# Performance work log

Hardware: AMD Instinct MI355X
Metric: run time of the kernel (lower is better)

Reference implementation:

```python
import jax, jax.numpy as jnp
import numpy as np

N_NODES = 100000
N_EDGES = 1000000
IN_DIM = 128
HID = 128
OUT_DIM = 40


def setup_inputs() -> dict:
    key = jax.random.key(0)
    ks = jax.random.split(key, 16)
    x = jax.random.normal(ks[0], (N_NODES, IN_DIM), dtype=jnp.float32)
    edge_index = jax.random.randint(ks[1], (2, N_EDGES), 0, N_NODES, dtype=jnp.int64)
    s = 0.05
    # GAT layer 1 (in->hid, heads=1, concat=True)
    W1 = jax.random.normal(ks[2], (HID, IN_DIM), jnp.float32) * s
    b1 = jnp.zeros((HID,), jnp.float32)
    att1 = jax.random.normal(ks[3], (1, 2 * HID), jnp.float32) * s
    bias1 = jnp.zeros((HID,), jnp.float32)
    # GAT layer 2 (hid->hid)
    W2 = jax.random.normal(ks[4], (HID, HID), jnp.float32) * s
    b2 = jnp.zeros((HID,), jnp.float32)
    att2 = jax.random.normal(ks[5], (1, 2 * HID), jnp.float32) * s
    bias2 = jnp.zeros((HID,), jnp.float32)
    # post_mp: Linear(hid,hid) -> Dropout -> Linear(hid,out)
    Wp1 = jax.random.normal(ks[6], (HID, HID), jnp.float32) * s
    bp1 = jnp.zeros((HID,), jnp.float32)
    Wp2 = jax.random.normal(ks[7], (OUT_DIM, HID), jnp.float32) * s
    bp2 = jnp.zeros((OUT_DIM,), jnp.float32)
    return dict(x=x, edge_index=edge_index, W1=W1, b1=b1, att1=att1, bias1=bias1,
                W2=W2, b2=b2, att2=att2, bias2=bias2,
                Wp1=Wp1, bp1=bp1, Wp2=Wp2, bp2=bp2)


def gat_layer(x, src, dst, W, b, att, bias, n_nodes):
    # x: [N, Fin] -> h: [N, C] (heads=1, concat=True)
    h = x @ W.T + b
    C = h.shape[1]
    att_i, att_j = att[0, :C], att[0, C:]  # split: first half pairs with x_i (dst), second with x_j (src)
    # per-node scalar projections, then gather per edge (avoids [E,2C] concat)
    e = (h @ att_i)[dst] + (h @ att_j)[src]  # [E]
    e = jnp.where(e > 0, e, 0.2 * e)  # leaky_relu(0.2)
    # segment softmax over destination nodes
    m = jax.ops.segment_max(e, dst, num_segments=n_nodes)
    ex = jnp.exp(e - m[dst])
    denom = jax.ops.segment_sum(ex, dst, num_segments=n_nodes)
    alpha = ex / denom[dst]
    out = jax.ops.segment_sum(h[src] * alpha[:, None], dst, num_segments=n_nodes)
    return out + bias


def reference(x, edge_index, W1, b1, att1, bias1, W2, b2, att2, bias2, Wp1, bp1, Wp2, bp2):
    src, dst = edge_index[0], edge_index[1]
    n = x.shape[0]
    h = jax.nn.relu(gat_layer(x, src, dst, W1, b1, att1, bias1, n))  # dropout p=0 -> identity
    h = jax.nn.relu(gat_layer(h, src, dst, W2, b2, att2, bias2, n))
    y = (h @ Wp1.T + bp1) @ Wp2.T + bp2  # post_mp (eval: dropout identity)
    return jax.nn.log_softmax(y, axis=1)
```

## Files before the change

### kernel.cpp

```cpp
#include <hip/hip_runtime.h>

#define N_NODES 100000
#define N_EDGES 1000000
#define HID 128
#define OUT_DIM 40
#define CSR_W 64
#define CUR_STRIDE 16
#define GEMM_TILES 1563
#define G2_TILES 782
#define PROJ_TILES 1563
#define EDGE_BLK 977
#define WC_BLK 21

typedef __attribute__((ext_vector_type(8))) short bf16x8;
typedef __attribute__((ext_vector_type(4))) float f32x4;

__device__ inline unsigned short f2bf(float f) {
    unsigned u = __float_as_uint(f);
    u += 0x7fffu + ((u >> 16) & 1u);
    return (unsigned short)(u >> 16);
}
__device__ inline float bf2f(unsigned short u) {
    return __uint_as_float(((unsigned)u) << 16);
}

__device__ inline float4 ld4(const float* p) { return *(const float4*)p; }
__device__ inline float4 ld4(const unsigned short* p) {
    ushort4 u = *(const ushort4*)p;
    return make_float4(bf2f(u.x), bf2f(u.y), bf2f(u.z), bf2f(u.w));
}

__global__ __launch_bounds__(256) void zero_kernel(float4* __restrict__ p, int n4) {
    int i = blockIdx.x * 256 + threadIdx.x;
    int stride = gridDim.x * 256;
    float4 z = make_float4(0.f, 0.f, 0.f, 0.f);
    for (; i < n4; i += stride) p[i] = z;
}

#define LDA 136
template<typename AT>
__device__ __forceinline__ void gemm_tile_body(
    int tile, const AT* __restrict__ A, const float* __restrict__ W,
    const float* __restrict__ out_bias, const float* __restrict__ in_bias,
    int relu_in, const float* __restrict__ att,
    unsigned short* __restrict__ Cb, float* __restrict__ hi, float* __restrict__ hj,
    int n_rows, unsigned short* As, unsigned short* Ws)
{
    const int t = threadIdx.x;
    const int row0 = tile * 64;

    for (int i = 0; i < 8; i++) {
        int lin = t + i * 256;
        int r = lin >> 5;
        int k = (lin & 31) * 4;
        int gr = row0 + r;
        float4 av = make_float4(0.f, 0.f, 0.f, 0.f);
        if (gr < n_rows) av = ld4(A + (size_t)gr * HID + k);
        if (in_bias) {
            av.x += in_bias[k + 0]; av.y += in_bias[k + 1];
            av.z += in_bias[k + 2]; av.w += in_bias[k + 3];
            if (relu_in) {
                av.x = fmaxf(av.x, 0.f); av.y = fmaxf(av.y, 0.f);
                av.z = fmaxf(av.z, 0.f); av.w = fmaxf(av.w, 0.f);
            }
        }
        ushort4 bv;
        bv.x = f2bf(av.x); bv.y = f2bf(av.y); bv.z = f2bf(av.z); bv.w = f2bf(av.w);
        *(ushort4*)(&As[r * LDA + k]) = bv;
    }
    for (int i = 0; i < 16; i++) {
        int lin = t + i * 256;
        int r = lin >> 5;
        int k = (lin & 31) * 4;
        float4 wv = *(const float4*)(W + (size_t)r * HID + k);
        ushort4 bv;
        bv.x = f2bf(wv.x); bv.y = f2bf(wv.y); bv.z = f2bf(wv.z); bv.w = f2bf(wv.w);
        *(ushort4*)(&Ws[r * LDA + k]) = bv;
    }
    __syncthreads();

    const int wave = t >> 6, lane = t & 63;
    const int lrow = lane & 15, quad = lane >> 4;
    const int wrow = wave * 16;

    f32x4 acc[8];
    #pragma unroll
    for (int ni = 0; ni < 8; ni++) acc[ni] = (f32x4){0.f, 0.f, 0.f, 0.f};

    #pragma unroll
    for (int ks = 0; ks < 4; ks++) {
        const int kb = ks * 32 + quad * 8;
        bf16x8 af = *(bf16x8*)(&As[(wrow + lrow) * LDA + kb]);
        #pragma unroll
        for (int ni = 0; ni < 8; ni++) {
            bf16x8 bfr = *(bf16x8*)(&Ws[(ni * 16 + lrow) * LDA + kb]);
            acc[ni] = __builtin_amdgcn_mfma_f32_16x16x32_bf16(af, bfr, acc[ni], 0, 0, 0);
        }
    }

    float pi[4] = {0.f, 0.f, 0.f, 0.f}, pj[4] = {0.f, 0.f, 0.f, 0.f};
    const int rbase = row0 + wrow + quad * 4;
    #pragma unroll
    for (int ni = 0; ni < 8; ni++) {
        const int col = ni * 16 + lrow;
        const float bo = out_bias[col];
        const float ai = att[col], aj = att[HID + col];
        #pragma unroll
        for (int r = 0; r < 4; r++) {
            float v = acc[ni][r] + bo;
            int gr = rbase + r;
            if (gr < n_rows) Cb[(size_t)gr * HID + col] = f2bf(v);
            pi[r] = fmaf(v, ai, pi[r]);
            pj[r] = fmaf(v, aj, pj[r]);
        }
    }
    #pragma unroll
    for (int o = 1; o < 16; o <<= 1) {
        #pragma unroll
        for (int r = 0; r < 4; r++) {
            pi[r] += __shfl_xor(pi[r], o);
            pj[r] += __shfl_xor(pj[r], o);
        }
    }
    if (lrow == 0) {
        #pragma unroll
        for (int r = 0; r < 4; r++) {
            int gr = rbase + r;
            if (gr < n_rows) { hi[gr] = pi[r]; hj[gr] = pj[r]; }
        }
    }
}

__global__ __launch_bounds__(256) void combined_prep(
    const float* __restrict__ x, const float* __restrict__ W1,
    const float* __restrict__ b1, const float* __restrict__ att1,
    const float* __restrict__ Wp1, const float* __restrict__ bp1,
    const float* __restrict__ Wp2, const float* __restrict__ bp2,
    const int* __restrict__ src, const int* __restrict__ dst,
    unsigned* __restrict__ cursor, int* __restrict__ csr,
    unsigned short* __restrict__ hbuf, float* __restrict__ hi, float* __restrict__ hj,
    float* __restrict__ Wc, float* __restrict__ bc)
{
    __shared__ unsigned short As[64 * LDA];
    __shared__ unsigned short Ws[128 * LDA];
    const int b = blockIdx.x, g = b >> 3, r = b & 7;

    if (r < 3) {
        const int eid = g * 3 + r;
        if (eid >= EDGE_BLK) return;
        int e = eid * 1024 + threadIdx.x;
        #pragma unroll
        for (int j = 0; j < 4; j++, e += 256) {
            if (e < N_EDGES) {
                int d = dst[e], s = src[e];
                unsigned p = atomicAdd(&cursor[d << 4], 1u);
                if (p < CSR_W) __builtin_nontemporal_store(s, &csr[(d << 6) + p]);
            }
        }
        return;
    }
    const int oid = g * 5 + (r - 3);
    if (oid < WC_BLK) {
        int t = oid * 256 + threadIdx.x;
        if (t < OUT_DIM * HID) {
            int o = t >> 7, k = t & 127;
            float s = 0.f;
            for (int j = 0; j < HID; j++) s = fmaf(Wp2[o * HID + j], Wp1[j * HID + k], s);
            Wc[t] = s;
        } else if (t < OUT_DIM * HID + OUT_DIM) {
            int o = t - OUT_DIM * HID;
            float s = bp2[o];
            for (int j = 0; j < HID; j++) s = fmaf(Wp2[o * HID + j], bp1[j], s);
            bc[o] = s;
        }
        return;
    }
    const int tile = oid - WC_BLK;
    if (tile >= GEMM_TILES) return;
    gemm_tile_body<float>(tile, x, W1, b1, nullptr, 0, att1, hbuf, hi, hj, N_NODES, As, Ws);
}

__global__ __launch_bounds__(256) void gemm_mfma_b128(
    const unsigned short* __restrict__ A, const float* __restrict__ W,
    const float* __restrict__ out_bias, const float* __restrict__ in_bias,
    const float* __restrict__ att,
    unsigned short* __restrict__ Cb, float* __restrict__ hi, float* __restrict__ hj,
    int n_rows)
{
    __shared__ unsigned short As[128 * LDA];
    __shared__ unsigned short Ws[128 * LDA];
    const int t = threadIdx.x;
    const int row0 = blockIdx.x * 128;

    for (int i = 0; i < 16; i++) {
        int lin = t + i * 256;
        int r = lin >> 5;
        int k = (lin & 31) * 4;
        int gr = row0 + r;
        float4 av = make_float4(0.f, 0.f, 0.f, 0.f);
        if (gr < n_rows) av = ld4(A + (size_t)gr * HID + k);
        av.x = fmaxf(av.x + in_bias[k + 0], 0.f);
        av.y = fmaxf(av.y + in_bias[k + 1], 0.f);
        av.z = fmaxf(av.z + in_bias[k + 2], 0.f);
        av.w = fmaxf(av.w + in_bias[k + 3], 0.f);
        ushort4 bv;
        bv.x = f2bf(av.x); bv.y = f2bf(av.y); bv.z = f2bf(av.z); bv.w = f2bf(av.w);
        *(ushort4*)(&As[r * LDA + k]) = bv;
    }
    for (int i = 0; i < 16; i++) {
        int lin = t + i * 256;
        int r = lin >> 5;
        int k = (lin & 31) * 4;
        float4 wv = *(const float4*)(W + (size_t)r * HID + k);
        ushort4 bv;
        bv.x = f2bf(wv.x); bv.y = f2bf(wv.y); bv.z = f2bf(wv.z); bv.w = f2bf(wv.w);
        *(ushort4*)(&Ws[r * LDA + k]) = bv;
    }
    __syncthreads();

    const int wave = t >> 6, lane = t & 63;
    const int lrow = lane & 15, quad = lane >> 4;

    f32x4 acc[2][8];
    #pragma unroll
    for (int mt = 0; mt < 2; mt++)
        #pragma unroll
        for (int ni = 0; ni < 8; ni++) acc[mt][ni] = (f32x4){0.f, 0.f, 0.f, 0.f};

    #pragma unroll
    for (int ks = 0; ks < 4; ks++) {
        const int kb = ks * 32 + quad * 8;
        bf16x8 af0 = *(bf16x8*)(&As[(wave * 32 + lrow) * LDA + kb]);
        bf16x8 af1 = *(bf16x8*)(&As[(wave * 32 + 16 + lrow) * LDA + kb]);
        #pragma unroll
        for (int ni = 0; ni < 8; ni++) {
            bf16x8 bfr = *(bf16x8*)(&Ws[(ni * 16 + lrow) * LDA + kb]);
            acc[0][ni] = __builtin_amdgcn_mfma_f32_16x16x32_bf16(af0, bfr, acc[0][ni], 0, 0, 0);
            acc[1][ni] = __builtin_amdgcn_mfma_f32_16x16x32_bf16(af1, bfr, acc[1][ni], 0, 0, 0);
        }
    }

    #pragma unroll
    for (int mt = 0; mt < 2; mt++) {
        float pi[4] = {0.f, 0.f, 0.f, 0.f}, pj[4] = {0.f, 0.f, 0.f, 0.f};
        const int rbase = row0 + wave * 32 + mt * 16 + quad * 4;
        #pragma unroll
        for (int ni = 0; ni < 8; ni++) {
            const int col = ni * 16 + lrow;
            const float bo = out_bias[col];
            const float ai = att[col], aj = att[HID + col];
            #pragma unroll
            for (int r = 0; r < 4; r++) {
                float v = acc[mt][ni][r] + bo;
                int gr = rbase + r;
                if (gr < n_rows) Cb[(size_t)gr * HID + col] = f2bf(v);
                pi[r] = fmaf(v, ai, pi[r]);
                pj[r] = fmaf(v, aj, pj[r]);
            }
        }
        #pragma unroll
        for (int o = 1; o < 16; o <<= 1) {
            #pragma unroll
            for (int r = 0; r < 4; r++) {
                pi[r] += __shfl_xor(pi[r], o);
                pj[r] += __shfl_xor(pj[r], o);
            }
        }
        if (lrow == 0) {
            #pragma unroll
            for (int r = 0; r < 4; r++) {
                int gr = rbase + r;
                if (gr < n_rows) { hi[gr] = pi[r]; hj[gr] = pj[r]; }
            }
        }
    }
}

__global__ __launch_bounds__(256) void fused_gat(
    const unsigned* __restrict__ cursor, const int* __restrict__ csr,
    const unsigned short* __restrict__ hb,
    const float* __restrict__ hi, const float* __restrict__ hj,
    unsigned short* __restrict__ out)
{
    const int wave = threadIdx.x >> 6;
    const int lane = threadIdx.x & 63;
    const int d = blockIdx.x * 4 + wave;
    if (d >= N_NODES) return;
    unsigned deg = cursor[d << 4];
    if (deg > CSR_W) deg = CSR_W;
    const int cnt = (int)deg;
    const float hid = hi[d];
    const int base = d << 6;

    int sv = 0;
    float ev = -INFINITY;
    if (lane < cnt) {
        sv = csr[base + lane];
        float e = hid + hj[sv];
        ev = e > 0.f ? e : 0.2f * e;
    }
    float m = ev;
    #pragma unroll
    for (int o = 32; o; o >>= 1) m = fmaxf(m, __shfl_xor(m, o));
    const float exv = (lane < cnt) ? __expf(ev - m) : 0.f;
    float denom = exv;
    #pragma unroll
    for (int o = 32; o; o >>= 1) denom += __shfl_xor(denom, o);

    float accx = 0.f, accy = 0.f;
    const int co = lane * 2;
    int i = 0;
    for (; i + 4 <= cnt; i += 4) {
        const int s0 = __shfl(sv, i),     s1 = __shfl(sv, i + 1);
        const int s2 = __shfl(sv, i + 2), s3 = __shfl(sv, i + 3);
        const float w0 = __shfl(exv, i),     w1 = __shfl(exv, i + 1);
        const float w2 = __shfl(exv, i + 2), w3 = __shfl(exv, i + 3);
        const ushort2 u0 = *(const ushort2*)(hb + (size_t)s0 * HID + co);
        const ushort2 u1 = *(const ushort2*)(hb + (size_t)s1 * HID + co);
        const ushort2 u2 = *(const ushort2*)(hb + (size_t)s2 * HID + co);
        const ushort2 u3 = *(const ushort2*)(hb + (size_t)s3 * HID + co);
        accx = fmaf(w0, bf2f(u0.x), accx); accy = fmaf(w0, bf2f(u0.y), accy);
        accx = fmaf(w1, bf2f(u1.x), accx); accy = fmaf(w1, bf2f(u1.y), accy);
        accx = fmaf(w2, bf2f(u2.x), accx); accy = fmaf(w2, bf2f(u2.y), accy);
        accx = fmaf(w3, bf2f(u3.x), accx); accy = fmaf(w3, bf2f(u3.y), accy);
    }
    for (; i < cnt; i++) {
        const int s = __shfl(sv, i);
        const float w = __shfl(exv, i);
        const ushort2 u = *(const ushort2*)(hb + (size_t)s * HID + co);
        accx = fmaf(w, bf2f(u.x), accx);
        accy = fmaf(w, bf2f(u.y), accy);
    }
    const float inv = cnt ? 1.f / denom : 0.f;
    ushort2 o2;
    o2.x = f2bf(accx * inv);
    o2.y = f2bf(accy * inv);
    *(ushort2*)(out + (size_t)d * HID + co) = o2;
}

__global__ __launch_bounds__(256) void final_proj_mfma(
    const unsigned short* __restrict__ agg, const float* __restrict__ bias2,
    const float* __restrict__ Wc, const float* __restrict__ bc,
    float* __restrict__ out)
{
    __shared__ unsigned short As[64 * LDA];
    __shared__ unsigned short Ws[48 * LDA];
    const int t = threadIdx.x;
    const int node0 = blockIdx.x * 64;

    for (int i = 0; i < 5; i++) {
        int lin = t + i * 256;
        int r = lin >> 5;
        int k = (lin & 31) * 4;
        float4 wv = *(const float4*)(Wc + (size_t)r * HID + k);
        ushort4 bv;
        bv.x = f2bf(wv.x); bv.y = f2bf(wv.y); bv.z = f2bf(wv.z); bv.w = f2bf(wv.w);
        *(ushort4*)(&Ws[r * LDA + k]) = bv;
    }
    {
        int r = 40 + (t >> 5);
        int k = (t & 31) * 4;
        ushort4 z; z.x = 0; z.y = 0; z.z = 0; z.w = 0;
        *(ushort4*)(&Ws[r * LDA + k]) = z;
    }
    for (int i = 0; i < 8; i++) {
        int lin = t + i * 256;
        int r = lin >> 5;
        int k = (lin & 31) * 4;
        int gr = node0 + r;
        float4 v = make_float4(0.f, 0.f, 0.f, 0.f);
        if (gr < N_NODES) v = ld4(agg + (size_t)gr * HID + k);
        v.x = fmaxf(v.x + bias2[k + 0], 0.f);
        v.y = fmaxf(v.y + bias2[k + 1], 0.f);
        v.z = fmaxf(v.z + bias2[k + 2], 0.f);
        v.w = fmaxf(v.w + bias2[k + 3], 0.f);
        ushort4 bv;
        bv.x = f2bf(v.x); bv.y = f2bf(v.y); bv.z = f2bf(v.z); bv.w = f2bf(v.w);
        *(ushort4*)(&As[r * LDA + k]) = bv;
    }
    __syncthreads();

    const int wave = t >> 6, lane = t & 63;
    const int lrow = lane & 15, quad = lane >> 4;
    const int wrow = wave * 16;

    f32x4 acc[3];
    #pragma unroll
    for (int nt = 0; nt < 3; nt++) acc[nt] = (f32x4){0.f, 0.f, 0.f, 0.f};

    #pragma unroll
    for (int ks = 0; ks < 4; ks++) {
        const int kb = ks * 32 + quad * 8;
        bf16x8 af = *(bf16x8*)(&As[(wrow + lrow) * LDA + kb]);
        #pragma unroll
        for (int nt = 0; nt < 3; nt++) {
            bf16x8 bfr = *(bf16x8*)(&Ws[(nt * 16 + lrow) * LDA + kb]);
            acc[nt] = __builtin_amdgcn_mfma_f32_16x16x32_bf16(af, bfr, acc[nt], 0, 0, 0);
        }
    }

    int cols[3]; float bcv[3]; bool valid[3];
    #pragma unroll
    for (int nt = 0; nt < 3; nt++) {
        cols[nt] = nt * 16 + lrow;
        valid[nt] = cols[nt] < OUT_DIM;
        bcv[nt] = valid[nt] ? bc[cols[nt]] : 0.f;
    }
    const int rbase = node0 + wrow + quad * 4;
    #pragma unroll
    for (int r = 0; r < 4; r++) {
        float v[3];
        float mx = -INFINITY;
        #pragma unroll
        for (int nt = 0; nt < 3; nt++) {
            v[nt] = acc[nt][r] + bcv[nt];
            if (valid[nt]) mx = fmaxf(mx, v[nt]);
        }
        #pragma unroll
        for (int o = 1; o < 16; o <<= 1) mx = fmaxf(mx, __shfl_xor(mx, o));
        float s = 0.f;
        #pragma unroll
        for (int nt = 0; nt < 3; nt++)
            if (valid[nt]) s += __expf(v[nt] - mx);
        #pragma unroll
        for (int o = 1; o < 16; o <<= 1) s += __shfl_xor(s, o);
        const float lse = mx + __logf(s);
        const int node = rbase + r;
        if (node < N_NODES) {
            #pragma unroll
            for (int nt = 0; nt < 3; nt++)
                if (valid[nt]) out[(size_t)node * OUT_DIM + cols[nt]] = v[nt] - lse;
        }
    }
}

extern "C" void kernel_launch(void* const* d_in, const int* in_sizes, int n_in,
                              void* d_out, int out_size, void* d_ws, size_t ws_size,
                              hipStream_t stream)
{
    const float* x     = (const float*)d_in[0];
    const int*   ei    = (const int*)d_in[1];
    const float* W1    = (const float*)d_in[2];
    const float* b1    = (const float*)d_in[3];
    const float* att1  = (const float*)d_in[4];
    const float* bias1 = (const float*)d_in[5];
    const float* W2    = (const float*)d_in[6];
    const float* b2    = (const float*)d_in[7];
    const float* att2  = (const float*)d_in[8];
    const float* bias2 = (const float*)d_in[9];
    const float* Wp1   = (const float*)d_in[10];
    const float* bp1   = (const float*)d_in[11];
    const float* Wp2   = (const float*)d_in[12];
    const float* bp2   = (const float*)d_in[13];
    float* out = (float*)d_out;

    const int* src = ei;
    const int* dst = ei + N_EDGES;

    char* ws = (char*)d_ws;
    unsigned short* hbuf = (unsigned short*)ws;
    unsigned short* aggb = hbuf + (size_t)N_NODES * HID;
    float* hi      = (float*)(aggb + (size_t)N_NODES * HID);
    float* hj      = hi + N_NODES;
    unsigned* cursor = (unsigned*)(hj + N_NODES);
    int* csr       = (int*)(cursor + (size_t)N_NODES * CUR_STRIDE);
    float* Wc      = (float*)(csr + (size_t)N_NODES * CSR_W);
    float* bc      = Wc + OUT_DIM * HID;

    const int prep_blocks = 326 * 8;

    zero_kernel<<<512, 256, 0, stream>>>((float4*)cursor, N_NODES * CUR_STRIDE / 4);

    combined_prep<<<prep_blocks, 256, 0, stream>>>(
        x, W1, b1, att1, Wp1, bp1, Wp2, bp2, src, dst,
        cursor, csr, hbuf, hi, hj, Wc, bc);

    fused_gat<<<N_NODES / 4, 256, 0, stream>>>(cursor, csr, hbuf, hi, hj, aggb);

    gemm_mfma_b128<<<G2_TILES, 256, 0, stream>>>(aggb, W2, b2, bias1, att2, hbuf, hi, hj, N_NODES);
    fused_gat<<<N_NODES / 4, 256, 0, stream>>>(cursor, csr, hbuf, hi, hj, aggb);

    final_proj_mfma<<<PROJ_TILES, 256, 0, stream>>>(aggb, bias2, Wc, bc, out);
}
```

Before: 319.8 us.

## Pre-convert weights to bf16 once and read B fragments from global; fuse bias+relu into aggregation

Weights W1, W2 and the fused post-MP matrix are converted to bf16 once, in an extended zero kernel and in the prep stage, instead of every GEMM block converting fp32 weights into shared memory. MFMA B fragments are then loaded straight from global/L2, and the weight shared-memory buffers are dropped, which lowers LDS use and may raise occupancy. Bias plus ReLU is moved into the GAT aggregation epilogue, so the following GEMMs load bf16 activations with plain 16-byte copies. The risk is that per-fragment global loads of B replace cheap LDS reads and may raise latency.

```diff
diff --git a/kernel.cpp b/kernel.cpp
--- a/kernel.cpp
+++ b/kernel.cpp
@@ -10,7 +10,7 @@
 #define G2_TILES 782
 #define PROJ_TILES 1563
 #define EDGE_BLK 977
-#define WC_BLK 21
+#define WC_BLK 25
 
 typedef __attribute__((ext_vector_type(8))) short bf16x8;
 typedef __attribute__((ext_vector_type(4))) float f32x4;
@@ -25,26 +25,40 @@
 }
 
 __device__ inline float4 ld4(const float* p) { return *(const float4*)p; }
-__device__ inline float4 ld4(const unsigned short* p) {
-    ushort4 u = *(const ushort4*)p;
-    return make_float4(bf2f(u.x), bf2f(u.y), bf2f(u.z), bf2f(u.w));
-}
-
-__global__ __launch_bounds__(256) void zero_kernel(float4* __restrict__ p, int n4) {
-    int i = blockIdx.x * 256 + threadIdx.x;
-    int stride = gridDim.x * 256;
-    float4 z = make_float4(0.f, 0.f, 0.f, 0.f);
-    for (; i < n4; i += stride) p[i] = z;
+
+__global__ __launch_bounds__(256) void zero_conv_kernel(
+    float4* __restrict__ p, int n4,
+    const float* __restrict__ W1, const float* __restrict__ W2,
+    unsigned short* __restrict__ W1b, unsigned short* __restrict__ W2b)
+{
+    if (blockIdx.x < 512) {
+        int i = blockIdx.x * 256 + threadIdx.x;
+        const int stride = 512 * 256;
+        float4 z = make_float4(0.f, 0.f, 0.f, 0.f);
+        for (; i < n4; i += stride) p[i] = z;
+        return;
+    }
+    const int L = (blockIdx.x - 512) * 256 + threadIdx.x;
+    const int e = L * 8;
+    const float* s;
+    unsigned short* d;
+    if (e < HID * HID) { s = W1 + e; d = W1b + e; }
+    else               { s = W2 + (e - HID * HID); d = W2b + (e - HID * HID); }
+    float4 a = *(const float4*)s;
+    float4 b = *(const float4*)(s + 4);
+    ushort4 u0, u1;
+    u0.x = f2bf(a.x); u0.y = f2bf(a.y); u0.z = f2bf(a.z); u0.w = f2bf(a.w);
+    u1.x = f2bf(b.x); u1.y = f2bf(b.y); u1.z = f2bf(b.z); u1.w = f2bf(b.w);
+    *(ushort4*)d = u0;
+    *(ushort4*)(d + 4) = u1;
 }
 
 #define LDA 136
-template<typename AT>
-__device__ __forceinline__ void gemm_tile_body(
-    int tile, const AT* __restrict__ A, const float* __restrict__ W,
-    const float* __restrict__ out_bias, const float* __restrict__ in_bias,
-    int relu_in, const float* __restrict__ att,
+__device__ __forceinline__ void gemm_tile_body_f32(
+    int tile, const float* __restrict__ A, const unsigned short* __restrict__ Wb,
+    const float* __restrict__ out_bias, const float* __restrict__ att,
     unsigned short* __restrict__ Cb, float* __restrict__ hi, float* __restrict__ hj,
-    int n_rows, unsigned short* As, unsigned short* Ws)
+    int n_rows, unsigned short* As)
 {
     const int t = threadIdx.x;
     const int row0 = tile * 64;
@@ -56,27 +70,10 @@
         int gr = row0 + r;
         float4 av = make_float4(0.f, 0.f, 0.f, 0.f);
         if (gr < n_rows) av = ld4(A + (size_t)gr * HID + k);
-        if (in_bias) {
-            av.x += in_bias[k + 0]; av.y += in_bias[k + 1];
-            av.z += in_bias[k + 2]; av.w += in_bias[k + 3];
-            if (relu_in) {
-                av.x = fmaxf(av.x, 0.f); av.y = fmaxf(av.y, 0.f);
-                av.z = fmaxf(av.z, 0.f); av.w = fmaxf(av.w, 0.f);
-            }
-        }
         ushort4 bv;
         bv.x = f2bf(av.x); bv.y = f2bf(av.y); bv.z = f2bf(av.z); bv.w = f2bf(av.w);
         *(ushort4*)(&As[r * LDA + k]) = bv;
     }
-    for (int i = 0; i < 16; i++) {
-        int lin = t + i * 256;
-        int r = lin >> 5;
-        int k = (lin & 31) * 4;
-        float4 wv = *(const float4*)(W + (size_t)r * HID + k);
-        ushort4 bv;
-        bv.x = f2bf(wv.x); bv.y = f2bf(wv.y); bv.z = f2bf(wv.z); bv.w = f2bf(wv.w);
-        *(ushort4*)(&Ws[r * LDA + k]) = bv;
-    }
     __syncthreads();
 
     const int wave = t >> 6, lane = t & 63;
@@ -93,7 +90,7 @@
         bf16x8 af = *(bf16x8*)(&As[(wrow + lrow) * LDA + kb]);
         #pragma unroll
         for (int ni = 0; ni < 8; ni++) {
-            bf16x8 bfr = *(bf16x8*)(&Ws[(ni * 16 + lrow) * LDA + kb]);
+            bf16x8 bfr = *(const bf16x8*)(Wb + (size_t)(ni * 16 + lrow) * HID + kb);
             acc[ni] = __builtin_amdgcn_mfma_f32_16x16x32_bf16(af, bfr, acc[ni], 0, 0, 0);
         }
     }
@@ -132,17 +129,16 @@
 }
 
 __global__ __launch_bounds__(256) void combined_prep(
-    const float* __restrict__ x, const float* __restrict__ W1,
+    const float* __restrict__ x, const unsigned short* __restrict__ W1b,
     const float* __restrict__ b1, const float* __restrict__ att1,
     const float* __restrict__ Wp1, const float* __restrict__ bp1,
     const float* __restrict__ Wp2, const float* __restrict__ bp2,
     const int* __restrict__ src, const int* __restrict__ dst,
     unsigned* __restrict__ cursor, int* __restrict__ csr,
     unsigned short* __restrict__ hbuf, float* __restrict__ hi, float* __restrict__ hj,
-    float* __restrict__ Wc, float* __restrict__ bc)
+    unsigned short* __restrict__ Wcb, float* __restrict__ bc)
 {
     __shared__ unsigned short As[64 * LDA];
-    __shared__ unsigned short Ws[128 * LDA];
     const int b = blockIdx.x, g = b >> 3, r = b & 7;
 
     if (r < 3) {
@@ -166,9 +162,11 @@
             int o = t >> 7, k = t & 127;
             float s = 0.f;
             for (int j = 0; j < HID; j++) s = fmaf(Wp2[o * HID + j], Wp1[j * HID + k], s);
-            Wc[t] = s;
-        } else if (t < OUT_DIM * HID + OUT_DIM) {
-            int o = t - OUT_DIM * HID;
+            Wcb[t] = f2bf(s);
+        } else if (t < 48 * HID) {
+            Wcb[t] = 0;
+        } else if (t < 48 * HID + OUT_DIM) {
+            int o = t - 48 * HID;
             float s = bp2[o];
             for (int j = 0; j < HID; j++) s = fmaf(Wp2[o * HID + j], bp1[j], s);
             bc[o] = s;
@@ -177,44 +175,27 @@
     }
     const int tile = oid - WC_BLK;
     if (tile >= GEMM_TILES) return;
-    gemm_tile_body<float>(tile, x, W1, b1, nullptr, 0, att1, hbuf, hi, hj, N_NODES, As, Ws);
+    gemm_tile_body_f32(tile, x, W1b, b1, att1, hbuf, hi, hj, N_NODES, As);
 }
 
 __global__ __launch_bounds__(256) void gemm_mfma_b128(
-    const unsigned short* __restrict__ A, const float* __restrict__ W,
-    const float* __restrict__ out_bias, const float* __restrict__ in_bias,
-    const float* __restrict__ att,
+    const unsigned short* __restrict__ A, const unsigned short* __restrict__ Wb,
+    const float* __restrict__ out_bias, const float* __restrict__ att,
     unsigned short* __restrict__ Cb, float* __restrict__ hi, float* __restrict__ hj,
     int n_rows)
 {
     __shared__ unsigned short As[128 * LDA];
-    __shared__ unsigned short Ws[128 * LDA];
     const int t = threadIdx.x;
     const int row0 = blockIdx.x * 128;
 
-    for (int i = 0; i < 16; i++) {
+    for (int i = 0; i < 8; i++) {
         int lin = t + i * 256;
-        int r = lin >> 5;
-        int k = (lin & 31) * 4;
+        int r = lin >> 4;
+        int k = (lin & 15) * 8;
         int gr = row0 + r;
-        float4 av = make_float4(0.f, 0.f, 0.f, 0.f);
-        if (gr < n_rows) av = ld4(A + (size_t)gr * HID + k);
-        av.x = fmaxf(av.x + in_bias[k + 0], 0.f);
-        av.y = fmaxf(av.y + in_bias[k + 1], 0.f);
-        av.z = fmaxf(av.z + in_bias[k + 2], 0.f);
-        av.w = fmaxf(av.w + in_bias[k + 3], 0.f);
-        ushort4 bv;
-        bv.x = f2bf(av.x); bv.y = f2bf(av.y); bv.z = f2bf(av.z); bv.w = f2bf(av.w);
-        *(ushort4*)(&As[r * LDA + k]) = bv;
-    }
-    for (int i = 0; i < 16; i++) {
-        int lin = t + i * 256;
-        int r = lin >> 5;
-        int k = (lin & 31) * 4;
-        float4 wv = *(const float4*)(W + (size_t)r * HID + k);
-        ushort4 bv;
-        bv.x = f2bf(wv.x); bv.y = f2bf(wv.y); bv.z = f2bf(wv.z); bv.w = f2bf(wv.w);
-        *(ushort4*)(&Ws[r * LDA + k]) = bv;
+        bf16x8 v = (bf16x8){0, 0, 0, 0, 0, 0, 0, 0};
+        if (gr < n_rows) v = *(const bf16x8*)(A + (size_t)gr * HID + k);
+        *(bf16x8*)(&As[r * LDA + k]) = v;
     }
     __syncthreads();
 
@@ -234,7 +215,7 @@
         bf16x8 af1 = *(bf16x8*)(&As[(wave * 32 + 16 + lrow) * LDA + kb]);
         #pragma unroll
         for (int ni = 0; ni < 8; ni++) {
-            bf16x8 bfr = *(bf16x8*)(&Ws[(ni * 16 + lrow) * LDA + kb]);
+            bf16x8 bfr = *(const bf16x8*)(Wb + (size_t)(ni * 16 + lrow) * HID + kb);
             acc[0][ni] = __builtin_amdgcn_mfma_f32_16x16x32_bf16(af0, bfr, acc[0][ni], 0, 0, 0);
             acc[1][ni] = __builtin_amdgcn_mfma_f32_16x16x32_bf16(af1, bfr, acc[1][ni], 0, 0, 0);
         }
@@ -280,6 +261,7 @@
     const unsigned* __restrict__ cursor, const int* __restrict__ csr,
     const unsigned short* __restrict__ hb,
     const float* __restrict__ hi, const float* __restrict__ hj,
+    const float* __restrict__ bias,
     unsigned short* __restrict__ out)
 {
     const int wave = threadIdx.x >> 6;
@@ -332,51 +314,30 @@
         accy = fmaf(w, bf2f(u.y), accy);
     }
     const float inv = cnt ? 1.f / denom : 0.f;
+    const float2 bv = *(const float2*)(bias + co);
     ushort2 o2;
-    o2.x = f2bf(accx * inv);
-    o2.y = f2bf(accy * inv);
+    o2.x = f2bf(fmaxf(fmaf(accx, inv, bv.x), 0.f));
+    o2.y = f2bf(fmaxf(fmaf(accy, inv, bv.y), 0.f));
     *(ushort2*)(out + (size_t)d * HID + co) = o2;
 }
 
 __global__ __launch_bounds__(256) void final_proj_mfma(
-    const unsigned short* __restrict__ agg, const float* __restrict__ bias2,
-    const float* __restrict__ Wc, const float* __restrict__ bc,
+    const unsigned short* __restrict__ agg,
+    const unsigned short* __restrict__ Wcb, const float* __restrict__ bc,
     float* __restrict__ out)
 {
     __shared__ unsigned short As[64 * LDA];
-    __shared__ unsigned short Ws[48 * LDA];
     const int t = threadIdx.x;
     const int node0 = blockIdx.x * 64;
 
-    for (int i = 0; i < 5; i++) {
+    for (int i = 0; i < 4; i++) {
         int lin = t + i * 256;
-        int r = lin >> 5;
-        int k = (lin & 31) * 4;
-        float4 wv = *(const float4*)(Wc + (size_t)r * HID + k);
-        ushort4 bv;
-        bv.x = f2bf(wv.x); bv.y = f2bf(wv.y); bv.z = f2bf(wv.z); bv.w = f2bf(wv.w);
-        *(ushort4*)(&Ws[r * LDA + k]) = bv;
-    }
-    {
-        int r = 40 + (t >> 5);
-        int k = (t & 31) * 4;
-        ushort4 z; z.x = 0; z.y = 0; z.z = 0; z.w = 0;
-        *(ushort4*)(&Ws[r * LDA + k]) = z;
-    }
-    for (int i = 0; i < 8; i++) {
-        int lin = t + i * 256;
-        int r = lin >> 5;
-        int k = (lin & 31) * 4;
+        int r = lin >> 4;
+        int k = (lin & 15) * 8;
         int gr = node0 + r;
-        float4 v = make_float4(0.f, 0.f, 0.f, 0.f);
-        if (gr < N_NODES) v = ld4(agg + (size_t)gr * HID + k);
-        v.x = fmaxf(v.x + bias2[k + 0], 0.f);
-        v.y = fmaxf(v.y + bias2[k + 1], 0.f);
-        v.z = fmaxf(v.z + bias2[k + 2], 0.f);
-        v.w = fmaxf(v.w + bias2[k + 3], 0.f);
-        ushort4 bv;
-        bv.x = f2bf(v.x); bv.y = f2bf(v.y); bv.z = f2bf(v.z); bv.w = f2bf(v.w);
-        *(ushort4*)(&As[r * LDA + k]) = bv;
+        bf16x8 v = (bf16x8){0, 0, 0, 0, 0, 0, 0, 0};
+        if (gr < N_NODES) v = *(const bf16x8*)(agg + (size_t)gr * HID + k);
+        *(bf16x8*)(&As[r * LDA + k]) = v;
     }
     __syncthreads();
 
@@ -394,7 +355,7 @@
         bf16x8 af = *(bf16x8*)(&As[(wrow + lrow) * LDA + kb]);
         #pragma unroll
         for (int nt = 0; nt < 3; nt++) {
-            bf16x8 bfr = *(bf16x8*)(&Ws[(nt * 16 + lrow) * LDA + kb]);
+            bf16x8 bfr = *(const bf16x8*)(Wcb + (size_t)(nt * 16 + lrow) * HID + kb);
             acc[nt] = __builtin_amdgcn_mfma_f32_16x16x32_bf16(af, bfr, acc[nt], 0, 0, 0);
         }
     }
@@ -464,21 +425,24 @@
     float* hj      = hi + N_NODES;
     unsigned* cursor = (unsigned*)(hj + N_NODES);
     int* csr       = (int*)(cursor + (size_t)N_NODES * CUR_STRIDE);
-    float* Wc      = (float*)(csr + (size_t)N_NODES * CSR_W);
-    float* bc      = Wc + OUT_DIM * HID;
+    unsigned short* Wcb = (unsigned short*)(csr + (size_t)N_NODES * CSR_W);
+    unsigned short* W1b = Wcb + 48 * HID;
+    unsigned short* W2b = W1b + HID * HID;
+    float* bc      = (float*)(W2b + HID * HID);
 
     const int prep_blocks = 326 * 8;
 
-    zero_kernel<<<512, 256, 0, stream>>>((float4*)cursor, N_NODES * CUR_STRIDE / 4);
+    zero_conv_kernel<<<528, 256, 0, stream>>>(
+        (float4*)cursor, N_NODES * CUR_STRIDE / 4, W1, W2, W1b, W2b);
 
     combined_prep<<<prep_blocks, 256, 0, stream>>>(
-        x, W1, b1, att1, Wp1, bp1, Wp2, bp2, src, dst,
-        cursor, csr, hbuf, hi, hj, Wc, bc);
-
-    fused_gat<<<N_NODES / 4, 256, 0, stream>>>(cursor, csr, hbuf, hi, hj, aggb);
-
-    gemm_mfma_b128<<<G2_TILES, 256, 0, stream>>>(aggb, W2, b2, bias1, att2, hbuf, hi, hj, N_NODES);
-    fused_gat<<<N_NODES / 4, 256, 0, stream>>>(cursor, csr, hbuf, hi, hj, aggb);
-
-    final_proj_mfma<<<PROJ_TILES, 256, 0, stream>>>(aggb, bias2, Wc, bc, out);
-}
+        x, W1b, b1, att1, Wp1, bp1, Wp2, bp2, src, dst,
+        cursor, csr, hbuf, hi, hj, Wcb, bc);
+
+    fused_gat<<<N_NODES / 4, 256, 0, stream>>>(cursor, csr, hbuf, hi, hj, bias1, aggb);
+
+    gemm_mfma_b128<<<G2_TILES, 256, 0, stream>>>(aggb, W2b, b2, att2, hbuf, hi, hj, N_NODES);
+    fused_gat<<<N_NODES / 4, 256, 0, stream>>>(cursor, csr, hbuf, hi, hj, bias2, aggb);
+
+    final_proj_mfma<<<PROJ_TILES, 256, 0, stream>>>(aggb, Wcb, bc, out);
+}
```

Result: slower. 343.3 us (+7.3%).
